# Kernel optimization log

Hardware: AMD Instinct MI355X
Metric: run time of the kernel (lower is better)

The kernel has to match this reference:

```python
import jax, jax.numpy as jnp
import numpy as np

EMD = 768
HEADS = 8
HEAD_DIM = EMD // HEADS


def setup_inputs() -> dict:
    key = jax.random.key(0)
    ks = jax.random.split(key, 9)
    s = 0.02
    x = jax.random.normal(ks[0], (4, 2048, EMD), dtype=jnp.float32)
    # torch nn.Linear weights: (out_features, in_features)
    Wq = jax.random.normal(ks[1], (EMD, EMD), dtype=jnp.float32) * s
    bq = jnp.zeros((EMD,), dtype=jnp.float32)
    Wk = jax.random.normal(ks[2], (EMD, EMD), dtype=jnp.float32) * s
    bk = jnp.zeros((EMD,), dtype=jnp.float32)
    Wv = jax.random.normal(ks[3], (EMD, EMD), dtype=jnp.float32) * s
    bv = jnp.zeros((EMD,), dtype=jnp.float32)
    Wo = jax.random.normal(ks[4], (EMD, EMD), dtype=jnp.float32) * s
    bo = jnp.zeros((EMD,), dtype=jnp.float32)
    return {"x": x, "Wq": Wq, "bq": bq, "Wk": Wk, "bk": bk,
            "Wv": Wv, "bv": bv, "Wo": Wo, "bo": bo}


def _split_heads(t):
    # [b, n, emd] -> [b, h, n, d]
    b, n, _ = t.shape
    return t.reshape(b, n, HEADS, HEAD_DIM).transpose(0, 2, 1, 3)


def reference(x, Wq, bq, Wk, bk, Wv, bv, Wo, bo):
    q = _split_heads(x @ Wq.T + bq)  # [b,h,n,d]
    k = _split_heads(x @ Wk.T + bk)
    v = _split_heads(x @ Wv.T + bv)
    energy = jnp.einsum('bhqd,bhkd->bhqk', q, k)  # [b,h,n,n]
    # NOTE: the original module applies softmax over the HEADS axis (dim=1),
    # then divides by sqrt(emd_size). We replicate that exactly.
    scaling = jnp.asarray(EMD ** 0.5, dtype=energy.dtype)
    attention = jax.nn.softmax(energy, axis=1) / scaling
    out = jnp.einsum('bhqk,bhkd->bhqd', attention, v)  # [b,h,n,d]
    b, h, n, d = out.shape
    out = out.transpose(0, 2, 1, 3).reshape(b, n, h * d)  # [b,n,emd]
    return out @ Wo.T + bo
```

## Files before the change

### kernel.cpp

```cpp
#include <hip/hip_runtime.h>
#include <stdint.h>

typedef __bf16 bf16;
typedef __bf16 bf16x4 __attribute__((ext_vector_type(4)));
typedef __bf16 bf16x8 __attribute__((ext_vector_type(8)));
typedef float  fx4    __attribute__((ext_vector_type(4)));

#define MFMA16(a, b, c) __builtin_amdgcn_mfma_f32_16x16x32_bf16((a), (b), (c), 0, 0, 0)


__device__ __forceinline__ void barrier_nodrain() {
  __asm__ __volatile__("" ::: "memory");
  __builtin_amdgcn_s_waitcnt(0xC07F);
  __builtin_amdgcn_s_barrier();
  __asm__ __volatile__("" ::: "memory");
}

__device__ __forceinline__ void wait_vm6() {
  __asm__ __volatile__("" ::: "memory");
  __builtin_amdgcn_s_waitcnt(0x0F76);
  __asm__ __volatile__("" ::: "memory");
}
__device__ __forceinline__ void wait_lgkm0() {
  __asm__ __volatile__("" ::: "memory");
  __builtin_amdgcn_s_waitcnt(0xC07F);
  __asm__ __volatile__("" ::: "memory");
}

__device__ __forceinline__ void gload_lds16(const void* g, void* l) {
  __builtin_amdgcn_global_load_lds(
      (const __attribute__((address_space(1))) void*)g,
      (__attribute__((address_space(3))) void*)l, 16, 0, 0);
}

__global__ __launch_bounds__(256)
void cvt_x_kernel(const float* __restrict__ x, bf16* __restrict__ xb) {
  const int i = (blockIdx.x * 256 + threadIdx.x) * 4;
  float4 v = *(const float4*)&x[i];
  bf16x4 o;
  o[0] = (bf16)v.x; o[1] = (bf16)v.y; o[2] = (bf16)v.z; o[3] = (bf16)v.w;
  *(bf16x4*)&xb[i] = o;
}

__global__ __launch_bounds__(256)
void gemm_qkv(const bf16* __restrict__ A,
              const float* __restrict__ Wq, const float* __restrict__ Wk,
              const float* __restrict__ Wv,
              const float* __restrict__ bq, const float* __restrict__ bk,
              const float* __restrict__ bv,
              bf16* __restrict__ Qo, bf16* __restrict__ Ka,
              bf16* __restrict__ Va) {
  constexpr int K = 768;
  __shared__ __align__(16) bf16 As[128 * 32];
  __shared__ __align__(16) bf16 Bs[128 * 32];

  const int tid  = threadIdx.x;
  const int wave = tid >> 6;
  const int lane = tid & 63;
  const int l15  = lane & 15;
  const int q4   = lane >> 4;
  const int wr   = wave >> 1;
  const int wc   = wave & 1;
  const int sel  = blockIdx.x / 6;
  const int cb0  = (blockIdx.x % 6) * 128;
  const int rb0  = blockIdx.y * 128;

  const float* W   = (sel == 0) ? Wq : (sel == 1) ? Wk : Wv;
  const float* bia = (sel == 0) ? bq : (sel == 1) ? bk : bv;

  fx4 acc[4][4];
#pragma unroll
  for (int i = 0; i < 4; i++)
#pragma unroll
    for (int j = 0; j < 4; j++) acc[i][j] = (fx4){0.f, 0.f, 0.f, 0.f};

  for (int k0 = 0; k0 < K; k0 += 32) {
    for (int c = tid; c < 512; c += 256) {
      const int row = c >> 2;
      const int kc  = (c & 3) << 3;
      *(uint4*)&As[row * 32 + kc] =
          *(const uint4*)&A[(size_t)(rb0 + row) * K + k0 + kc];
      const float* sb = W + (size_t)(cb0 + row) * K + k0 + kc;
      bf16x8 pb;
#pragma unroll
      for (int t = 0; t < 8; t++) pb[t] = (bf16)sb[t];
      *(bf16x8*)&Bs[row * 32 + kc] = pb;
    }
    __syncthreads();

    bf16x8 a[4], b[4];
#pragma unroll
    for (int i = 0; i < 4; i++)
      a[i] = *(const bf16x8*)&As[(wr * 64 + i * 16 + l15) * 32 + q4 * 8];
#pragma unroll
    for (int j = 0; j < 4; j++)
      b[j] = *(const bf16x8*)&Bs[(wc * 64 + j * 16 + l15) * 32 + q4 * 8];
#pragma unroll
    for (int i = 0; i < 4; i++)
#pragma unroll
      for (int j = 0; j < 4; j++)
        acc[i][j] = MFMA16(a[i], b[j], acc[i][j]);
    __syncthreads();
  }

  const int cb = cb0 + wc * 64;
  const int rb = rb0 + wr * 64;
#pragma unroll
  for (int j = 0; j < 4; j++) {
    const int o  = cb + j * 16 + l15;
    const float bj = bia[o];
    const int hh = o / 96;
    const int dd = o - hh * 96;
#pragma unroll
    for (int i = 0; i < 4; i++) {
      const int r0 = rb + i * 16 + q4 * 4;
      if (sel == 2) {
        const int bb = r0 >> 11;
        const int n2 = r0 & 2047;
        const size_t flat =
            ((size_t)((bb * 8 + hh) * 64 + (n2 >> 5))) * 3072 +
            ((n2 >> 3) & 3) * 768 + dd * 8 + (n2 & 7);
        bf16x4 pk;
#pragma unroll
        for (int r = 0; r < 4; r++) pk[r] = (bf16)(acc[i][j][r] + bj);
        *(bf16x4*)&Va[flat] = pk;
      } else if (sel == 1) {
        const int u  = dd >> 3;
        const int de = dd & 7;
#pragma unroll
        for (int r = 0; r < 4; r++) {
          const int n  = r0 + r;
          const int bb = n >> 11;
          const int n2 = n & 2047;
          const size_t flat =
              ((size_t)((bb * 8 + hh) * 64 + (n2 >> 5))) * 3072 +
              u * 256 + (n2 & 31) * 8 + de;
          Ka[flat] = (bf16)(acc[i][j][r] + bj);
        }
      } else {
#pragma unroll
        for (int r = 0; r < 4; r++)
          Qo[(size_t)(r0 + r) * 768 + o] = (bf16)(acc[i][j][r] + bj);
      }
    }
  }
}

__global__ __launch_bounds__(256)
void gemm_o(const bf16* __restrict__ A, const float* __restrict__ W,
            const float* __restrict__ bias, float* __restrict__ C) {
  constexpr int K = 768;
  __shared__ __align__(16) bf16 As[128 * 32];
  __shared__ __align__(16) bf16 Bs[128 * 32];

  const int tid  = threadIdx.x;
  const int wave = tid >> 6;
  const int lane = tid & 63;
  const int l15  = lane & 15;
  const int q4   = lane >> 4;
  const int wr   = wave >> 1;
  const int wc   = wave & 1;
  const int rb0  = blockIdx.y * 128;
  const int cb0  = blockIdx.x * 128;

  fx4 acc[4][4];
#pragma unroll
  for (int i = 0; i < 4; i++)
#pragma unroll
    for (int j = 0; j < 4; j++) acc[i][j] = (fx4){0.f, 0.f, 0.f, 0.f};

  for (int k0 = 0; k0 < K; k0 += 32) {
    for (int c = tid; c < 512; c += 256) {
      const int row = c >> 2;
      const int kc  = (c & 3) << 3;
      *(uint4*)&As[row * 32 + kc] =
          *(const uint4*)&A[(size_t)(rb0 + row) * K + k0 + kc];
      const float* sb = W + (size_t)(cb0 + row) * K + k0 + kc;
      bf16x8 pb;
#pragma unroll
      for (int t = 0; t < 8; t++) pb[t] = (bf16)sb[t];
      *(bf16x8*)&Bs[row * 32 + kc] = pb;
    }
    __syncthreads();

    bf16x8 a[4], b[4];
#pragma unroll
    for (int i = 0; i < 4; i++)
      a[i] = *(const bf16x8*)&As[(wr * 64 + i * 16 + l15) * 32 + q4 * 8];
#pragma unroll
    for (int j = 0; j < 4; j++)
      b[j] = *(const bf16x8*)&Bs[(wc * 64 + j * 16 + l15) * 32 + q4 * 8];
#pragma unroll
    for (int i = 0; i < 4; i++)
#pragma unroll
      for (int j = 0; j < 4; j++)
        acc[i][j] = MFMA16(a[i], b[j], acc[i][j]);
    __syncthreads();
  }

  const int cb = cb0 + wc * 64;
  const int rb = rb0 + wr * 64;
#pragma unroll
  for (int j = 0; j < 4; j++) {
    const int o  = cb + j * 16 + l15;
    const float bj = bias[o];
#pragma unroll
    for (int i = 0; i < 4; i++) {
      const int r0 = rb + i * 16 + q4 * 4;
#pragma unroll
      for (int r = 0; r < 4; r++)
        C[(size_t)(r0 + r) * 768 + o] = acc[i][j][r] + bj;
    }
  }
}

__global__ __launch_bounds__(512, 1)
void attn_kernel(const bf16* Q, const bf16* __restrict__ Ka,
                 const bf16* __restrict__ Va, bf16* AO) {
  __shared__ __align__(16) bf16  Kbuf[8 * 3072];
  __shared__ __align__(16) bf16  Vbuf[8 * 3072];
  __shared__ __align__(16) float Ebuf[32 * 260];

  const int tid  = threadIdx.x;
  const int h    = tid >> 6;
  const int lane = tid & 63;
  const int l15  = lane & 15;
  const int q4   = lane >> 4;
  const int b    = blockIdx.x >> 6;
  const int qt   = blockIdx.x & 63;
  const int qrow0 = b * 2048 + qt * 32;

  bf16x8 aq[2][3];
#pragma unroll
  for (int i = 0; i < 2; i++)
#pragma unroll
    for (int c = 0; c < 3; c++)
      aq[i][c] = *(const bf16x8*)
          &Q[(size_t)(qrow0 + i * 16 + l15) * 768 + h * 96 + c * 32 + q4 * 8];

  fx4 o[2][6];
#pragma unroll
  for (int i = 0; i < 2; i++)
#pragma unroll
    for (int j = 0; j < 6; j++) o[i][j] = (fx4){0.f, 0.f, 0.f, 0.f};

  const bf16* Kt0 = Ka + (size_t)(b * 8 + h) * 64 * 3072;
  const bf16* Vt0 = Va + (size_t)(b * 8 + h) * 64 * 3072;
  bf16* Kl = &Kbuf[h * 3072];
  bf16* Vl = &Vbuf[h * 3072];

  auto stageK = [&](int kt) {
    const bf16* src = Kt0 + (size_t)kt * 3072 + lane * 8;
#pragma unroll
    for (int t = 0; t < 6; t++)
      gload_lds16(src + t * 512, Kl + t * 512);
  };
  auto stageV = [&](int kt) {
    const bf16* src = Vt0 + (size_t)kt * 3072 + lane * 8;
#pragma unroll
    for (int t = 0; t < 6; t++)
      gload_lds16(src + t * 512, Vl + t * 512);
  };

  stageK(0);
  stageV(0);

  for (int kt = 0; kt < 64; kt++) {
    const int kn = (kt + 1 < 64) ? kt + 1 : 63;

    wait_vm6();

    bf16x8 bk[2][3];
#pragma unroll
    for (int j = 0; j < 2; j++)
#pragma unroll
      for (int c = 0; c < 3; c++)
        bk[j][c] =
            *(const bf16x8*)&Kl[(c * 4 + q4) * 256 + (j * 16 + l15) * 8];

    wait_lgkm0();
    stageK(kn);

    fx4 e[2][2];
    e[0][0] = e[0][1] = e[1][0] = e[1][1] = (fx4){0.f, 0.f, 0.f, 0.f};
#pragma unroll
    for (int c = 0; c < 3; c++)
#pragma unroll
      for (int j = 0; j < 2; j++) {
        e[0][j] = MFMA16(aq[0][c], bk[j][c], e[0][j]);
        e[1][j] = MFMA16(aq[1][c], bk[j][c], e[1][j]);
      }

#pragma unroll
    for (int i = 0; i < 2; i++)
#pragma unroll
      for (int j = 0; j < 2; j++)
#pragma unroll
        for (int r = 0; r < 4; r++)
          Ebuf[(i * 16 + q4 * 4 + r) * 260 + h * 32 + j * 16 + l15] =
              e[i][j][r];
    barrier_nodrain();

#pragma unroll
    for (int pp = 0; pp < 2; pp++) {
      const int p = tid + pp * 512;
      const int q = p >> 5, k = p & 31;
      float* row = &Ebuf[q * 260 + k];
      float v[8];
#pragma unroll
      for (int hh = 0; hh < 8; hh++) v[hh] = row[hh * 32];
      float m = v[0];
#pragma unroll
      for (int hh = 1; hh < 8; hh++) m = fmaxf(m, v[hh]);
      float sm = 0.f;
#pragma unroll
      for (int hh = 0; hh < 8; hh++) { v[hh] = __expf(v[hh] - m); sm += v[hh]; }
      const float inv = 1.0f / (sm * 27.712812921102035f);
#pragma unroll
      for (int hh = 0; hh < 8; hh++) row[hh * 32] = v[hh] * inv;
    }
    barrier_nodrain();

    wait_vm6();

    bf16x8 bv[6];
#pragma unroll
    for (int j2 = 0; j2 < 6; j2++)
      bv[j2] = *(const bf16x8*)&Vl[q4 * 768 + (j2 * 16 + l15) * 8];

    bf16x8 ap[2];
#pragma unroll
    for (int i = 0; i < 2; i++) {
      const float* ps = &Ebuf[(i * 16 + l15) * 260 + h * 32 + q4 * 8];
      fx4 p0 = *(const fx4*)ps;
      fx4 p1 = *(const fx4*)(ps + 4);
      bf16x8 t;
      t[0] = (bf16)p0[0]; t[1] = (bf16)p0[1];
      t[2] = (bf16)p0[2]; t[3] = (bf16)p0[3];
      t[4] = (bf16)p1[0]; t[5] = (bf16)p1[1];
      t[6] = (bf16)p1[2]; t[7] = (bf16)p1[3];
      ap[i] = t;
    }

    wait_lgkm0();
    stageV(kn);

#pragma unroll
    for (int j2 = 0; j2 < 6; j2++) {
      o[0][j2] = MFMA16(ap[0], bv[j2], o[0][j2]);
      o[1][j2] = MFMA16(ap[1], bv[j2], o[1][j2]);
    }
  }

  __builtin_amdgcn_s_waitcnt(0x0070);

#pragma unroll
  for (int i = 0; i < 2; i++)
#pragma unroll
    for (int j2 = 0; j2 < 6; j2++)
#pragma unroll
      for (int r = 0; r < 4; r++)
        AO[(size_t)(qrow0 + i * 16 + q4 * 4 + r) * 768 + h * 96 + j2 * 16 + l15] =
            (bf16)(o[i][j2][r]);
}

extern "C" void kernel_launch(void* const* d_in, const int* in_sizes, int n_in,
                              void* d_out, int out_size, void* d_ws,
                              size_t ws_size, hipStream_t stream) {
  const float* x  = (const float*)d_in[0];
  const float* Wq = (const float*)d_in[1];
  const float* bq = (const float*)d_in[2];
  const float* Wk = (const float*)d_in[3];
  const float* bk = (const float*)d_in[4];
  const float* Wv = (const float*)d_in[5];
  const float* bv = (const float*)d_in[6];
  const float* Wo = (const float*)d_in[7];
  const float* bo = (const float*)d_in[8];

  const size_t MN = (size_t)8192 * 768;
  bf16* xb = (bf16*)d_out;
  bf16* Ka = xb + MN;
  bf16* Q  = (bf16*)d_ws;
  bf16* Va = Q + MN;
  bf16* AO = Q;

  cvt_x_kernel<<<6144, 256, 0, stream>>>(x, xb);
  dim3 qkvgrid(18, 64);
  gemm_qkv<<<qkvgrid, 256, 0, stream>>>(xb, Wq, Wk, Wv, bq, bk, bv, Q, Ka, Va);
  attn_kernel<<<256, 512, 0, stream>>>(Q, Ka, Va, AO);
  dim3 ogrid(6, 64);
  gemm_o<<<ogrid, 256, 0, stream>>>(AO, Wo, bo, (float*)d_out);
}
```

Measured before the change: 319.2 us.

## Double-buffer A tiles via direct global-to-LDS loads in projection GEMMs

Measured after the change: 316.4 us. Within noise of the previous version (-0.9%).

```diff
diff --git a/kernel.cpp b/kernel.cpp
--- a/kernel.cpp
+++ b/kernel.cpp
@@ -51,7 +51,7 @@
               bf16* __restrict__ Qo, bf16* __restrict__ Ka,
               bf16* __restrict__ Va) {
   constexpr int K = 768;
-  __shared__ __align__(16) bf16 As[128 * 32];
+  __shared__ __align__(16) bf16 As[2][128 * 32];
   __shared__ __align__(16) bf16 Bs[128 * 32];
 
   const int tid  = threadIdx.x;
@@ -68,30 +68,53 @@
   const float* W   = (sel == 0) ? Wq : (sel == 1) ? Wk : Wv;
   const float* bia = (sel == 0) ? bq : (sel == 1) ? bk : bv;
 
+  const int ar0 = tid >> 2,         akc0 = (tid & 3) << 3;
+  const int ar1 = ar0 + 64,         akc1 = akc0;
+
   fx4 acc[4][4];
 #pragma unroll
   for (int i = 0; i < 4; i++)
 #pragma unroll
     for (int j = 0; j < 4; j++) acc[i][j] = (fx4){0.f, 0.f, 0.f, 0.f};
 
-  for (int k0 = 0; k0 < K; k0 += 32) {
-    for (int c = tid; c < 512; c += 256) {
-      const int row = c >> 2;
-      const int kc  = (c & 3) << 3;
-      *(uint4*)&As[row * 32 + kc] =
-          *(const uint4*)&A[(size_t)(rb0 + row) * K + k0 + kc];
-      const float* sb = W + (size_t)(cb0 + row) * K + k0 + kc;
-      bf16x8 pb;
-#pragma unroll
-      for (int t = 0; t < 8; t++) pb[t] = (bf16)sb[t];
-      *(bf16x8*)&Bs[row * 32 + kc] = pb;
-    }
-    __syncthreads();
+  gload_lds16(&A[(size_t)(rb0 + ar0) * K + akc0], &As[0][wave * 512]);
+  gload_lds16(&A[(size_t)(rb0 + ar1) * K + akc1], &As[0][(wave + 4) * 512]);
+
+  int cur = 0;
+  for (int k0 = 0; k0 < K; k0 += 32, cur ^= 1) {
+    const float* wp0 = W + (size_t)(cb0 + ar0) * K + k0 + akc0;
+    const float* wp1 = W + (size_t)(cb0 + ar1) * K + k0 + akc1;
+    const float4 b0a = *(const float4*)wp0;
+    const float4 b0b = *(const float4*)(wp0 + 4);
+    const float4 b1a = *(const float4*)wp1;
+    const float4 b1b = *(const float4*)(wp1 + 4);
+    __asm__ __volatile__("" ::: "memory");
+
+    const int kn = (k0 + 32 < K) ? k0 + 32 : k0;
+    gload_lds16(&A[(size_t)(rb0 + ar0) * K + kn + akc0],
+                &As[cur ^ 1][wave * 512]);
+    gload_lds16(&A[(size_t)(rb0 + ar1) * K + kn + akc1],
+                &As[cur ^ 1][(wave + 4) * 512]);
+    __asm__ __volatile__("" ::: "memory");
+
+    bf16x8 pb0, pb1;
+    pb0[0] = (bf16)b0a.x; pb0[1] = (bf16)b0a.y;
+    pb0[2] = (bf16)b0a.z; pb0[3] = (bf16)b0a.w;
+    pb0[4] = (bf16)b0b.x; pb0[5] = (bf16)b0b.y;
+    pb0[6] = (bf16)b0b.z; pb0[7] = (bf16)b0b.w;
+    pb1[0] = (bf16)b1a.x; pb1[1] = (bf16)b1a.y;
+    pb1[2] = (bf16)b1a.z; pb1[3] = (bf16)b1a.w;
+    pb1[4] = (bf16)b1b.x; pb1[5] = (bf16)b1b.y;
+    pb1[6] = (bf16)b1b.z; pb1[7] = (bf16)b1b.w;
+    *(bf16x8*)&Bs[ar0 * 32 + akc0] = pb0;
+    *(bf16x8*)&Bs[ar1 * 32 + akc1] = pb1;
+
+    barrier_nodrain();
 
     bf16x8 a[4], b[4];
 #pragma unroll
     for (int i = 0; i < 4; i++)
-      a[i] = *(const bf16x8*)&As[(wr * 64 + i * 16 + l15) * 32 + q4 * 8];
+      a[i] = *(const bf16x8*)&As[cur][(wr * 64 + i * 16 + l15) * 32 + q4 * 8];
 #pragma unroll
     for (int j = 0; j < 4; j++)
       b[j] = *(const bf16x8*)&Bs[(wc * 64 + j * 16 + l15) * 32 + q4 * 8];
@@ -100,7 +123,8 @@
 #pragma unroll
       for (int j = 0; j < 4; j++)
         acc[i][j] = MFMA16(a[i], b[j], acc[i][j]);
-    __syncthreads();
+
+    barrier_nodrain();
   }
 
   const int cb = cb0 + wc * 64;
@@ -150,7 +174,7 @@
 void gemm_o(const bf16* __restrict__ A, const float* __restrict__ W,
             const float* __restrict__ bias, float* __restrict__ C) {
   constexpr int K = 768;
-  __shared__ __align__(16) bf16 As[128 * 32];
+  __shared__ __align__(16) bf16 As[2][128 * 32];
   __shared__ __align__(16) bf16 Bs[128 * 32];
 
   const int tid  = threadIdx.x;
@@ -163,30 +187,53 @@
   const int rb0  = blockIdx.y * 128;
   const int cb0  = blockIdx.x * 128;
 
+  const int ar0 = tid >> 2,         akc0 = (tid & 3) << 3;
+  const int ar1 = ar0 + 64,         akc1 = akc0;
+
   fx4 acc[4][4];
 #pragma unroll
   for (int i = 0; i < 4; i++)
 #pragma unroll
     for (int j = 0; j < 4; j++) acc[i][j] = (fx4){0.f, 0.f, 0.f, 0.f};
 
-  for (int k0 = 0; k0 < K; k0 += 32) {
-    for (int c = tid; c < 512; c += 256) {
-      const int row = c >> 2;
-      const int kc  = (c & 3) << 3;
-      *(uint4*)&As[row * 32 + kc] =
-          *(const uint4*)&A[(size_t)(rb0 + row) * K + k0 + kc];
-      const float* sb = W + (size_t)(cb0 + row) * K + k0 + kc;
-      bf16x8 pb;
-#pragma unroll
-      for (int t = 0; t < 8; t++) pb[t] = (bf16)sb[t];
-      *(bf16x8*)&Bs[row * 32 + kc] = pb;
-    }
-    __syncthreads();
+  gload_lds16(&A[(size_t)(rb0 + ar0) * K + akc0], &As[0][wave * 512]);
+  gload_lds16(&A[(size_t)(rb0 + ar1) * K + akc1], &As[0][(wave + 4) * 512]);
+
+  int cur = 0;
+  for (int k0 = 0; k0 < K; k0 += 32, cur ^= 1) {
+    const float* wp0 = W + (size_t)(cb0 + ar0) * K + k0 + akc0;
+    const float* wp1 = W + (size_t)(cb0 + ar1) * K + k0 + akc1;
+    const float4 b0a = *(const float4*)wp0;
+    const float4 b0b = *(const float4*)(wp0 + 4);
+    const float4 b1a = *(const float4*)wp1;
+    const float4 b1b = *(const float4*)(wp1 + 4);
+    __asm__ __volatile__("" ::: "memory");
+
+    const int kn = (k0 + 32 < K) ? k0 + 32 : k0;
+    gload_lds16(&A[(size_t)(rb0 + ar0) * K + kn + akc0],
+                &As[cur ^ 1][wave * 512]);
+    gload_lds16(&A[(size_t)(rb0 + ar1) * K + kn + akc1],
+                &As[cur ^ 1][(wave + 4) * 512]);
+    __asm__ __volatile__("" ::: "memory");
+
+    bf16x8 pb0, pb1;
+    pb0[0] = (bf16)b0a.x; pb0[1] = (bf16)b0a.y;
+    pb0[2] = (bf16)b0a.z; pb0[3] = (bf16)b0a.w;
+    pb0[4] = (bf16)b0b.x; pb0[5] = (bf16)b0b.y;
+    pb0[6] = (bf16)b0b.z; pb0[7] = (bf16)b0b.w;
+    pb1[0] = (bf16)b1a.x; pb1[1] = (bf16)b1a.y;
+    pb1[2] = (bf16)b1a.z; pb1[3] = (bf16)b1a.w;
+    pb1[4] = (bf16)b1b.x; pb1[5] = (bf16)b1b.y;
+    pb1[6] = (bf16)b1b.z; pb1[7] = (bf16)b1b.w;
+    *(bf16x8*)&Bs[ar0 * 32 + akc0] = pb0;
+    *(bf16x8*)&Bs[ar1 * 32 + akc1] = pb1;
+
+    barrier_nodrain();
 
     bf16x8 a[4], b[4];
 #pragma unroll
     for (int i = 0; i < 4; i++)
-      a[i] = *(const bf16x8*)&As[(wr * 64 + i * 16 + l15) * 32 + q4 * 8];
+      a[i] = *(const bf16x8*)&As[cur][(wr * 64 + i * 16 + l15) * 32 + q4 * 8];
 #pragma unroll
     for (int j = 0; j < 4; j++)
       b[j] = *(const bf16x8*)&Bs[(wc * 64 + j * 16 + l15) * 32 + q4 * 8];
@@ -195,7 +242,8 @@
 #pragma unroll
       for (int j = 0; j < 4; j++)
         acc[i][j] = MFMA16(a[i], b[j], acc[i][j]);
-    __syncthreads();
+
+    barrier_nodrain();
   }
 
   const int cb = cb0 + wc * 64;
```
